# Kernel tuning notes

Hardware: AMD Instinct MI355X
Metric: run time of the kernel (lower is better)

Reference implementation:

```python
import jax, jax.numpy as jnp
import numpy as np

# ---- grid / solver constants (from opt) ----
NZ, NX = 300, 400
NPML, NPAD = 32, 0
NZP = NZ + 2 * NPML + NPAD   # 364 padded depth
NXP = NX + 2 * NPML          # 464 padded width
NSTEPS = 200
NSHOTS = 2
DX = 0.01    # km (moduli scaled by 1e-6 => velocities in km/s)
DT = 0.001   # s
SRC_Z = NPML + 2
REC_Z = NPML + 2


def _pad_model(m):
    # edge-replicate into the CPML halo + bottom pad, as ft.padding does
    return jnp.pad(m, ((NPML, NPML + NPAD), (NPML, NPML)), mode='edge')


def _sponge():
    # smooth absorbing profile in the nPml halo (sponge approximation of CPML)
    i = np.arange(NZP, dtype=np.float32)
    j = np.arange(NXP, dtype=np.float32)
    dz = np.clip(np.maximum(NPML - i, i - (NZP - 1 - NPML - NPAD)), 0, NPML) / NPML
    dx_ = np.clip(np.maximum(NPML - j, j - (NXP - 1 - NPML)), 0, NPML) / NPML
    d = dz[:, None] ** 2 + dx_[None, :] ** 2
    return jnp.asarray(np.exp(-0.1 * d), dtype=jnp.float32)


# staggered-grid finite differences (zero outside the grid)
def _dxf(f):
    return (jnp.pad(f[:, 1:], ((0, 0), (0, 1))) - f) / DX

def _dxb(f):
    return (f - jnp.pad(f[:, :-1], ((0, 0), (1, 0)))) / DX

def _dzf(f):
    return (jnp.pad(f[1:, :], ((0, 1), (0, 0))) - f) / DX

def _dzb(f):
    return (f - jnp.pad(f[:-1, :], ((1, 0), (0, 0)))) / DX


def _propagate(lam, mu, rho, stf, src_x, damp):
    """Elastic velocity-stress FDTD for one shot. stf: [NSTEPS]. Returns recs [NSTEPS, NX]."""
    lam2mu = lam + 2.0 * mu
    dt_rho = DT / rho
    zero = jnp.zeros((NZP, NXP), jnp.float32)

    def step(carry, s):
        vx, vz, sxx, szz, sxz = carry
        vx = (vx + dt_rho * (_dxf(sxx) + _dzb(sxz))) * damp
        vz = (vz + dt_rho * (_dxb(sxz) + _dzf(szz))) * damp
        dvx_dx = _dxb(vx)
        dvz_dz = _dzb(vz)
        sxx = (sxx + DT * (lam2mu * dvx_dx + lam * dvz_dz)) * damp
        szz = (szz + DT * (lam * dvx_dx + lam2mu * dvz_dz)) * damp
        sxz = (sxz + DT * mu * (_dzf(vx) + _dxf(vz))) * damp
        # explosive source injected into normal stresses
        sxx = sxx.at[SRC_Z, src_x].add(s * DT)
        szz = szz.at[SRC_Z, src_x].add(s * DT)
        rec = vx[REC_Z, NPML:NPML + NX]  # surface receiver line
        return (vx, vz, sxx, szz, sxz), rec

    init = (zero, zero, zero, zero, zero)
    _, recs = jax.lax.scan(step, init, stf)
    return recs


def _forward(Vp, Vs, Den, Stf, Mask, Shot_ids):
    Vp_pad = _pad_model(Vp)
    Vs_pad = _pad_model(Vs)
    Den_pad = _pad_model(Den)
    # masked models: gradient flows only where Mask == 1
    Vp_m = Mask * Vp_pad + (1.0 - Mask) * jax.lax.stop_gradient(Vp_pad)
    Vs_m = Mask * Vs_pad + (1.0 - Mask) * jax.lax.stop_gradient(Vs_pad)
    Den_m = Mask * Den_pad + (1.0 - Mask) * jax.lax.stop_gradient(Den_pad)
    Lam = (Vp_m ** 2 - 2.0 * Vs_m ** 2) * Den_m / 1.0e6
    Mu = Vs_m ** 2 * Den_m / 1.0e6

    damp = _sponge()
    ids = Shot_ids.astype(jnp.int32)
    src_x = NPML + 20 + ids * ((NX - 40) // NSHOTS)  # per-shot source x position
    stf = Stf[ids]                                   # [nshots, NSTEPS]
    recs = jax.vmap(lambda s, sx: _propagate(Lam, Mu, Den_m, s, sx, damp))(stf, src_x)
    return 0.5 * jnp.sum(recs.astype(jnp.float32) ** 2)  # scalar misfit


def setup_inputs() -> dict:
    key = jax.random.key(0)
    k1, k2 = jax.random.split(key)
    Vp = 2000.0 + 1500.0 * jax.random.uniform(k1, (NZ, NX), jnp.float32)   # m/s
    Vs = Vp / 1.732
    Den = 2000.0 + 500.0 * jax.random.uniform(k2, (NZ, NX), jnp.float32)   # kg/m^3
    # Ricker wavelet source, f0 = 10 Hz, shared across shots
    t = jnp.arange(NSTEPS, dtype=jnp.float32) * DT - 0.1
    f0 = 10.0
    arg = (jnp.pi * f0 * t) ** 2
    ricker = (1.0 - 2.0 * arg) * jnp.exp(-arg)
    Stf = jnp.broadcast_to(ricker, (NSHOTS, NSTEPS)).astype(jnp.float32)
    Mask = jnp.ones((NZP, NXP), jnp.float32)
    Shot_ids = jnp.arange(NSHOTS, dtype=jnp.int32)
    return {"Vp": Vp, "Vs": Vs, "Den": Den, "Stf": Stf, "Mask": Mask,
            "Shot_ids": Shot_ids, "ngpu": 1}


def reference(Vp, Vs, Den, Stf, Mask, Shot_ids, ngpu):
    return _forward(Vp, Vs, Den, Stf, Mask, Shot_ids)
```

## Files before the change

kernel.cpp:

```cpp
#include <hip/hip_runtime.h>
#include <cmath>

typedef unsigned long long u64;

namespace {
constexpr int kNZ = 300, kNX = 400;
constexpr int kNPML = 32;
constexpr int kNZP = 364, kNXP = 464;
constexpr int kNSTEPS = 200, kNSHOTS = 2;
constexpr int kSRC_Z = 34, kREC_Z = 34;
constexpr float kDT = 0.001f;
constexpr float kINV_DX = 100.0f;

constexpr int kR = 4;
constexpr int kNSLAB = 92;
constexpr int kNB = kNSLAB - 1;
constexpr int kBlocks = kNSHOTS * kNSLAB;
constexpr int kThreads = 512;
constexpr int kPitch = 468;
constexpr int kFStride = kR * kPitch;

constexpr int kFlagStride = 32;
constexpr int kHaloBase = 16384;
constexpr int kHaloCount = 2 * kNSHOTS * kNB * 2 * 6 * kNXP;
constexpr int kPartOff = kHaloBase + kHaloCount;
}

__global__ __launch_bounds__(kThreads, 1) void fwi_sim_kernel(
    const float* __restrict__ Vp, const float* __restrict__ Vs,
    const float* __restrict__ Den, const float* __restrict__ Stf,
    const int* __restrict__ Shot_ids, float* __restrict__ ws,
    float* __restrict__ out) {
    __shared__ float L[4 * kFStride];
    float* Lvx  = L;
    float* Lvz  = L + kFStride;
    float* Lsxx = L + 2 * kFStride;
    float* Lsxz = L + 3 * kFStride;

    const int blk  = blockIdx.x;
    const int s    = blk / kNSLAB;
    const int slab = blk - s * kNSLAB;
    const int r0   = slab * kR;
    const int tid  = threadIdx.x;
    const bool active = tid < kNXP;
    const int lc = tid + 1;

    int*   flags = (int*)ws;
    float* halo  = ws + kHaloBase;
    u64*   part  = (u64*)(ws + kPartOff);

    for (int q = tid; q < 4 * kFStride; q += kThreads) L[q] = 0.0f;

    auto modAt = [&](int i, int j, float& dtr_, float& dmp_, float& lam_,
                     float& mu_, float& l2m_) {
        dtr_ = dmp_ = lam_ = mu_ = l2m_ = 0.0f;
        if (i >= 0 && i < kNZP && j >= 0 && j < kNXP) {
            int iz = i - kNPML; iz = iz < 0 ? 0 : (iz > kNZ - 1 ? kNZ - 1 : iz);
            int jx = j - kNPML; jx = jx < 0 ? 0 : (jx > kNX - 1 ? kNX - 1 : jx);
            const float vp  = Vp[iz * kNX + jx];
            const float vs  = Vs[iz * kNX + jx];
            const float rho = Den[iz * kNX + jx];
            const float m = vs * vs * rho * 1e-6f;
            const float l = (vp * vp - 2.0f * vs * vs) * rho * 1e-6f;
            const float sc = kDT * kINV_DX;
            float dz = fmaxf((float)(kNPML - i), (float)(i - (kNZP - 1 - kNPML)));
            dz = fminf(fmaxf(dz, 0.0f), (float)kNPML) * (1.0f / kNPML);
            float dxx = fmaxf((float)(kNPML - j), (float)(j - (kNXP - 1 - kNPML)));
            dxx = fminf(fmaxf(dxx, 0.0f), (float)kNPML) * (1.0f / kNPML);
            dmp_ = expf(-0.1f * (dz * dz + dxx * dxx));
            dtr_ = kDT / rho * kINV_DX;
            lam_ = l * sc;
            mu_  = m * sc;
            l2m_ = (l + 2.0f * m) * sc;
        }
    };
    float rdtr[kR], rdamp[kR], rlam[kR], rmu[kR], rl2m[kR];
    float dtrT = 0, dmpT = 0, dtrB = 0, dmpB = 0;
    if (active) {
#pragma unroll
        for (int r = 0; r < kR; ++r)
            modAt(r0 + r, tid, rdtr[r], rdamp[r], rlam[r], rmu[r], rl2m[r]);
        float d0, d1, d2;
        modAt(r0 - 1, tid, dtrT, dmpT, d0, d1, d2);
        modAt(r0 + kR, tid, dtrB, dmpB, d0, d1, d2);
    }

    const int id  = Shot_ids[s];
    const int sxp = kNPML + 20 + id * ((kNX - 40) / kNSHOTS);
    const float* stf = Stf + id * kNSTEPS;
    const int rsrc = kSRC_Z - r0;
    const int rrec = kREC_Z - r0;
    const bool isRecBlock = (rrec >= 0 && rrec < kR);
    const float srcm = (active && tid == sxp) ? 1.0f : 0.0f;
    const float recm = (active && (unsigned)(tid - kNPML) < (unsigned)kNX) ? 1.0f : 0.0f;

    const bool hasTop = (slab > 0);
    const bool hasBot = (slab < kNSLAB - 1);
    int* ftopw = hasTop ? &flags[((s * kNB + (slab - 1)) * 2 + 1) * kFlagStride] : nullptr;
    int* fbotw = hasBot ? &flags[((s * kNB + slab) * 2 + 0) * kFlagStride] : nullptr;
    int* ftopr = hasTop ? &flags[((s * kNB + (slab - 1)) * 2 + 0) * kFlagStride] : nullptr;
    int* fbotr = hasBot ? &flags[((s * kNB + slab) * 2 + 1) * kFlagStride] : nullptr;
    auto hbase = [&](int buf, int b, int dir) {
        return halo + ((((buf * kNSHOTS + s) * kNB + b) * 2 + dir) * 6) * kNXP;
    };

    float fvx[kR]  = {}, fvz[kR]  = {}, fsxx[kR] = {}, fszz[kR] = {}, fsxz[kR] = {};
    float rsum = 0.0f;
    __syncthreads();

    for (int t = 0; t < kNSTEPS; ++t) {
        const int rb = (t & 1) ^ 1;
        const int wb = t & 1;

        if (active) {
#pragma unroll
            for (int r = 1; r <= kR - 2; ++r) {
                const float sxxC = fsxx[r];
                const float sxzC = fsxz[r];
                const float szzC = fszz[r];
                const float sxxR = Lsxx[r * kPitch + lc + 1];
                const float sxzL = Lsxz[r * kPitch + lc - 1];
                const float nvx = (fvx[r] + rdtr[r] * ((sxxR - sxxC) + (sxzC - fsxz[r - 1]))) * rdamp[r];
                const float nvz = (fvz[r] + rdtr[r] * ((sxzC - sxzL) + (fszz[r + 1] - szzC))) * rdamp[r];
                fvx[r] = nvx;
                fvz[r] = nvz;
                Lvx[r * kPitch + lc] = nvx;
                Lvz[r * kPitch + lc] = nvz;
                if (r == rrec) rsum += recm * nvx * nvx;
            }
        }

        if (t > 0) {
            if (hasTop) {
                while (__hip_atomic_load(ftopr, __ATOMIC_RELAXED, __HIP_MEMORY_SCOPE_AGENT) < t) {}
            }
            if (hasBot) {
                while (__hip_atomic_load(fbotr, __ATOMIC_RELAXED, __HIP_MEMORY_SCOPE_AGENT) < t) {}
            }
        }

        float h_vxT = 0, h_vzT = 0, h_sxxT = 0, h_szzT = 0, h_sxzT = 0, h_sxz2T = 0;
        float h_sxxT_r = 0, h_sxzT_l = 0;
        float h_vxB = 0, h_vzB = 0, h_sxxB = 0, h_sxzB = 0, h_szzB = 0, h_szz2B = 0;
        float h_sxxB_r = 0, h_sxzB_l = 0;
        if (t > 0 && active && hasTop) {
            const float* hb = hbase(rb, slab - 1, 0);
            h_vxT   = __hip_atomic_load(hb + tid,             __ATOMIC_RELAXED, __HIP_MEMORY_SCOPE_AGENT);
            h_vzT   = __hip_atomic_load(hb + kNXP + tid,      __ATOMIC_RELAXED, __HIP_MEMORY_SCOPE_AGENT);
            h_sxxT  = __hip_atomic_load(hb + 2 * kNXP + tid,  __ATOMIC_RELAXED, __HIP_MEMORY_SCOPE_AGENT);
            h_szzT  = __hip_atomic_load(hb + 3 * kNXP + tid,  __ATOMIC_RELAXED, __HIP_MEMORY_SCOPE_AGENT);
            h_sxzT  = __hip_atomic_load(hb + 4 * kNXP + tid,  __ATOMIC_RELAXED, __HIP_MEMORY_SCOPE_AGENT);
            h_sxz2T = __hip_atomic_load(hb + 5 * kNXP + tid,  __ATOMIC_RELAXED, __HIP_MEMORY_SCOPE_AGENT);
            if (tid < kNXP - 1) h_sxxT_r = __hip_atomic_load(hb + 2 * kNXP + tid + 1, __ATOMIC_RELAXED, __HIP_MEMORY_SCOPE_AGENT);
            if (tid > 0)        h_sxzT_l = __hip_atomic_load(hb + 4 * kNXP + tid - 1, __ATOMIC_RELAXED, __HIP_MEMORY_SCOPE_AGENT);
        }
        if (t > 0 && active && hasBot) {
            const float* hb = hbase(rb, slab, 1);
            h_vxB   = __hip_atomic_load(hb + tid,             __ATOMIC_RELAXED, __HIP_MEMORY_SCOPE_AGENT);
            h_vzB   = __hip_atomic_load(hb + kNXP + tid,      __ATOMIC_RELAXED, __HIP_MEMORY_SCOPE_AGENT);
            h_sxxB  = __hip_atomic_load(hb + 2 * kNXP + tid,  __ATOMIC_RELAXED, __HIP_MEMORY_SCOPE_AGENT);
            h_sxzB  = __hip_atomic_load(hb + 3 * kNXP + tid,  __ATOMIC_RELAXED, __HIP_MEMORY_SCOPE_AGENT);
            h_szzB  = __hip_atomic_load(hb + 4 * kNXP + tid,  __ATOMIC_RELAXED, __HIP_MEMORY_SCOPE_AGENT);
            h_szz2B = __hip_atomic_load(hb + 5 * kNXP + tid,  __ATOMIC_RELAXED, __HIP_MEMORY_SCOPE_AGENT);
            if (tid < kNXP - 1) h_sxxB_r = __hip_atomic_load(hb + 2 * kNXP + tid + 1, __ATOMIC_RELAXED, __HIP_MEMORY_SCOPE_AGENT);
            if (tid > 0)        h_sxzB_l = __hip_atomic_load(hb + 3 * kNXP + tid - 1, __ATOMIC_RELAXED, __HIP_MEMORY_SCOPE_AGENT);
        }

        float nvxT = 0, nvzT = 0, nvxB = 0, nvzB = 0;
        if (active) {
            nvxT = (h_vxT + dtrT * ((h_sxxT_r - h_sxxT) + (h_sxzT - h_sxz2T))) * dmpT;
            nvzT = (h_vzT + dtrT * ((h_sxzT - h_sxzT_l) + (fszz[0] - h_szzT))) * dmpT;
            nvxB = (h_vxB + dtrB * ((h_sxxB_r - h_sxxB) + (h_sxzB - fsxz[kR - 1]))) * dmpB;
            nvzB = (h_vzB + dtrB * ((h_sxzB - h_sxzB_l) + (h_szz2B - h_szzB))) * dmpB;
            {
                const float sxxC = fsxx[0], sxzC = fsxz[0], szzC = fszz[0];
                const float sxxR = Lsxx[lc + 1];
                const float sxzL = Lsxz[lc - 1];
                const float nvx = (fvx[0] + rdtr[0] * ((sxxR - sxxC) + (sxzC - h_sxzT))) * rdamp[0];
                const float nvz = (fvz[0] + rdtr[0] * ((sxzC - sxzL) + (fszz[1] - szzC))) * rdamp[0];
                fvx[0] = nvx; fvz[0] = nvz;
                Lvx[lc] = nvx; Lvz[lc] = nvz;
                if (0 == rrec) rsum += recm * nvx * nvx;
            }
            {
                const int r = kR - 1;
                const float sxxC = fsxx[r], sxzC = fsxz[r], szzC = fszz[r];
                const float sxxR = Lsxx[r * kPitch + lc + 1];
                const float sxzL = Lsxz[r * kPitch + lc - 1];
                const float nvx = (fvx[r] + rdtr[r] * ((sxxR - sxxC) + (sxzC - fsxz[r - 1]))) * rdamp[r];
                const float nvz = (fvz[r] + rdtr[r] * ((sxzC - sxzL) + (h_szzB - szzC))) * rdamp[r];
                fvx[r] = nvx; fvz[r] = nvz;
                Lvx[r * kPitch + lc] = nvx; Lvz[r * kPitch + lc] = nvz;
                if (r == rrec) rsum += recm * nvx * nvx;
            }
        }
        __syncthreads();

        if (active) {
            const float sval = stf[t] * kDT;
#pragma unroll
            for (int r = 0; r < kR; ++r) {
                const float vxC = fvx[r];
                const float vzC = fvz[r];
                const float vxL = Lvx[r * kPitch + lc - 1];
                const float vzR = Lvz[r * kPitch + lc + 1];
                const float vzU = (r > 0) ? fvz[r - 1] : nvzT;
                const float vxD = (r < kR - 1) ? fvx[r + 1] : nvxB;
                const float dvx = vxC - vxL;
                const float dvz = vzC - vzU;
                float nsxx = (fsxx[r] + (rl2m[r] * dvx + rlam[r] * dvz)) * rdamp[r];
                float nszz = (fszz[r] + (rlam[r] * dvx + rl2m[r] * dvz)) * rdamp[r];
                float nsxz = (fsxz[r] + rmu[r] * ((vxD - vxC) + (vzR - vzC))) * rdamp[r];
                if (r == rsrc) { nsxx += srcm * sval; nszz += srcm * sval; }
                fsxx[r] = nsxx;
                fszz[r] = nszz;
                fsxz[r] = nsxz;
                Lsxx[r * kPitch + lc] = nsxx;
                Lsxz[r * kPitch + lc] = nsxz;
            }
            if (hasTop) {
                float* hb = hbase(wb, slab - 1, 1);
                __hip_atomic_store(hb + tid,            fvx[0],  __ATOMIC_RELAXED, __HIP_MEMORY_SCOPE_AGENT);
                __hip_atomic_store(hb + kNXP + tid,     fvz[0],  __ATOMIC_RELAXED, __HIP_MEMORY_SCOPE_AGENT);
                __hip_atomic_store(hb + 2 * kNXP + tid, fsxx[0], __ATOMIC_RELAXED, __HIP_MEMORY_SCOPE_AGENT);
                __hip_atomic_store(hb + 3 * kNXP + tid, fsxz[0], __ATOMIC_RELAXED, __HIP_MEMORY_SCOPE_AGENT);
                __hip_atomic_store(hb + 4 * kNXP + tid, fszz[0], __ATOMIC_RELAXED, __HIP_MEMORY_SCOPE_AGENT);
                __hip_atomic_store(hb + 5 * kNXP + tid, fszz[1], __ATOMIC_RELAXED, __HIP_MEMORY_SCOPE_AGENT);
            }
            if (hasBot) {
                float* hb = hbase(wb, slab, 0);
                __hip_atomic_store(hb + tid,            fvx[kR - 1],  __ATOMIC_RELAXED, __HIP_MEMORY_SCOPE_AGENT);
                __hip_atomic_store(hb + kNXP + tid,     fvz[kR - 1],  __ATOMIC_RELAXED, __HIP_MEMORY_SCOPE_AGENT);
                __hip_atomic_store(hb + 2 * kNXP + tid, fsxx[kR - 1], __ATOMIC_RELAXED, __HIP_MEMORY_SCOPE_AGENT);
                __hip_atomic_store(hb + 3 * kNXP + tid, fszz[kR - 1], __ATOMIC_RELAXED, __HIP_MEMORY_SCOPE_AGENT);
                __hip_atomic_store(hb + 4 * kNXP + tid, fsxz[kR - 1], __ATOMIC_RELAXED, __HIP_MEMORY_SCOPE_AGENT);
                __hip_atomic_store(hb + 5 * kNXP + tid, fsxz[kR - 2], __ATOMIC_RELAXED, __HIP_MEMORY_SCOPE_AGENT);
            }
        }
        __syncthreads();
        if (tid == 0 && hasTop) __hip_atomic_store(ftopw, t + 1, __ATOMIC_RELAXED, __HIP_MEMORY_SCOPE_AGENT);
        if (tid == 1 && hasBot) __hip_atomic_store(fbotw, t + 1, __ATOMIC_RELAXED, __HIP_MEMORY_SCOPE_AGENT);
    }

    for (int off = 32; off > 0; off >>= 1) rsum += __shfl_down(rsum, off, 64);
    __syncthreads();
    if ((tid & 63) == 0) L[tid >> 6] = rsum;
    __syncthreads();
    if (isRecBlock && tid == 0) {
        float tot = 0.0f;
#pragma unroll
        for (int w = 0; w < kThreads / 64; ++w) tot += L[w];
        const u64 word = ((u64)1 << 32) | (u64)__float_as_uint(tot);
        __hip_atomic_store(&part[s], word, __ATOMIC_RELAXED, __HIP_MEMORY_SCOPE_AGENT);
    }
    if (blk == 0 && tid == 0) {
        u64 v0, v1;
        do { v0 = __hip_atomic_load(&part[0], __ATOMIC_RELAXED, __HIP_MEMORY_SCOPE_AGENT); }
        while ((int)(v0 >> 32) < 1);
        do { v1 = __hip_atomic_load(&part[1], __ATOMIC_RELAXED, __HIP_MEMORY_SCOPE_AGENT); }
        while ((int)(v1 >> 32) < 1);
        out[0] = 0.5f * (__uint_as_float((unsigned)v0) + __uint_as_float((unsigned)v1));
    }
}

extern "C" void kernel_launch(void* const* d_in, const int* in_sizes, int n_in,
                              void* d_out, int out_size, void* d_ws, size_t ws_size,
                              hipStream_t stream) {
    const float* Vp  = (const float*)d_in[0];
    const float* Vs  = (const float*)d_in[1];
    const float* Den = (const float*)d_in[2];
    const float* Stf = (const float*)d_in[3];
    const int* Shot_ids = (const int*)d_in[5];
    float* out = (float*)d_out;
    float* ws  = (float*)d_ws;

    fwi_sim_kernel<<<kBlocks, kThreads, 0, stream>>>(Vp, Vs, Den, Stf,
                                                     Shot_ids, ws, out);
}
```

Baseline: 604.8 us.

## Overlap interior velocity update with halo publish and use lighter barriers

The interior-row velocity update for the next step now runs after the stress phase and before the flag publish, so it overlaps the latency of the halo stores. Boundary stress rows are computed first so halo stores issue earlier. __syncthreads is replaced by inline-asm barriers that wait only on LDS counters, with a vmcnt drain before the flags are signalled. The per-neighbour flag wait is also interleaved with that neighbour's halo loads. The risk is memory-ordering correctness, since the code relies on hand-written waitcnt plus relaxed atomics.

```diff
diff --git a/kernel.cpp b/kernel.cpp
--- a/kernel.cpp
+++ b/kernel.cpp
@@ -25,6 +25,42 @@
 constexpr int kHaloCount = 2 * kNSHOTS * kNB * 2 * 6 * kNXP;
 constexpr int kPartOff = kHaloBase + kHaloCount;
 }
+
+#define ALD(p)    __hip_atomic_load((p),       __ATOMIC_RELAXED, __HIP_MEMORY_SCOPE_AGENT)
+#define AST(p, v) __hip_atomic_store((p), (v), __ATOMIC_RELAXED, __HIP_MEMORY_SCOPE_AGENT)
+#define LDS_BAR() asm volatile("s_waitcnt lgkmcnt(0)\n\ts_barrier" ::: "memory")
+#define DRAIN_BAR() asm volatile("s_waitcnt vmcnt(0)\n\ts_barrier" ::: "memory")
+
+#define PRE_VEL()                                                              \
+  if (active) {                                                                \
+    _Pragma("unroll")                                                          \
+    for (int r = 1; r <= kR - 2; ++r) {                                        \
+      const float sxxC = fsxx[r], sxzC = fsxz[r], szzC = fszz[r];              \
+      const float sxxR = Lsxx[r * kPitch + lc + 1];                            \
+      const float sxzL = Lsxz[r * kPitch + lc - 1];                            \
+      const float nvx = (fvx[r] + rdtr[r] * ((sxxR - sxxC) + (sxzC - fsxz[r - 1]))) * rdamp[r]; \
+      const float nvz = (fvz[r] + rdtr[r] * ((sxzC - sxzL) + (fszz[r + 1] - szzC))) * rdamp[r]; \
+      fvx[r] = nvx; fvz[r] = nvz;                                              \
+      Lvx[r * kPitch + lc] = nvx; Lvz[r * kPitch + lc] = nvz;                  \
+      if (r == rrec) rsum += recm * nvx * nvx;                                 \
+    }                                                                          \
+  }
+
+#define STRESS_ROW(r, VZU, VXD)                                                \
+  {                                                                            \
+    const float vxC = fvx[r], vzC = fvz[r];                                    \
+    const float vxL = Lvx[(r) * kPitch + lc - 1];                              \
+    const float vzR = Lvz[(r) * kPitch + lc + 1];                              \
+    const float dvx = vxC - vxL;                                               \
+    const float dvz = vzC - (VZU);                                             \
+    float nsxx = (fsxx[r] + (rl2m[r] * dvx + rlam[r] * dvz)) * rdamp[r];       \
+    float nszz = (fszz[r] + (rlam[r] * dvx + rl2m[r] * dvz)) * rdamp[r];       \
+    float nsxz = (fsxz[r] + rmu[r] * (((VXD) - vxC) + (vzR - vzC))) * rdamp[r];\
+    if ((r) == rsrc) { nsxx += srcm * sval; nszz += srcm * sval; }             \
+    fsxx[r] = nsxx; fszz[r] = nszz; fsxz[r] = nsxz;                            \
+    Lsxx[(r) * kPitch + lc] = nsxx;                                            \
+    Lsxz[(r) * kPitch + lc] = nsxz;                                            \
+  }
 
 __global__ __launch_bounds__(kThreads, 1) void fwi_sim_kernel(
     const float* __restrict__ Vp, const float* __restrict__ Vs,
@@ -108,70 +144,51 @@
     float rsum = 0.0f;
     __syncthreads();
 
+    PRE_VEL()
+
     for (int t = 0; t < kNSTEPS; ++t) {
         const int rb = (t & 1) ^ 1;
         const int wb = t & 1;
-
-        if (active) {
-#pragma unroll
-            for (int r = 1; r <= kR - 2; ++r) {
-                const float sxxC = fsxx[r];
-                const float sxzC = fsxz[r];
-                const float szzC = fszz[r];
-                const float sxxR = Lsxx[r * kPitch + lc + 1];
-                const float sxzL = Lsxz[r * kPitch + lc - 1];
-                const float nvx = (fvx[r] + rdtr[r] * ((sxxR - sxxC) + (sxzC - fsxz[r - 1]))) * rdamp[r];
-                const float nvz = (fvz[r] + rdtr[r] * ((sxzC - sxzL) + (fszz[r + 1] - szzC))) * rdamp[r];
-                fvx[r] = nvx;
-                fvz[r] = nvz;
-                Lvx[r * kPitch + lc] = nvx;
-                Lvz[r * kPitch + lc] = nvz;
-                if (r == rrec) rsum += recm * nvx * nvx;
-            }
-        }
-
-        if (t > 0) {
-            if (hasTop) {
-                while (__hip_atomic_load(ftopr, __ATOMIC_RELAXED, __HIP_MEMORY_SCOPE_AGENT) < t) {}
-            }
-            if (hasBot) {
-                while (__hip_atomic_load(fbotr, __ATOMIC_RELAXED, __HIP_MEMORY_SCOPE_AGENT) < t) {}
-            }
-        }
 
         float h_vxT = 0, h_vzT = 0, h_sxxT = 0, h_szzT = 0, h_sxzT = 0, h_sxz2T = 0;
         float h_sxxT_r = 0, h_sxzT_l = 0;
         float h_vxB = 0, h_vzB = 0, h_sxxB = 0, h_sxzB = 0, h_szzB = 0, h_szz2B = 0;
         float h_sxxB_r = 0, h_sxzB_l = 0;
-        if (t > 0 && active && hasTop) {
-            const float* hb = hbase(rb, slab - 1, 0);
-            h_vxT   = __hip_atomic_load(hb + tid,             __ATOMIC_RELAXED, __HIP_MEMORY_SCOPE_AGENT);
-            h_vzT   = __hip_atomic_load(hb + kNXP + tid,      __ATOMIC_RELAXED, __HIP_MEMORY_SCOPE_AGENT);
-            h_sxxT  = __hip_atomic_load(hb + 2 * kNXP + tid,  __ATOMIC_RELAXED, __HIP_MEMORY_SCOPE_AGENT);
-            h_szzT  = __hip_atomic_load(hb + 3 * kNXP + tid,  __ATOMIC_RELAXED, __HIP_MEMORY_SCOPE_AGENT);
-            h_sxzT  = __hip_atomic_load(hb + 4 * kNXP + tid,  __ATOMIC_RELAXED, __HIP_MEMORY_SCOPE_AGENT);
-            h_sxz2T = __hip_atomic_load(hb + 5 * kNXP + tid,  __ATOMIC_RELAXED, __HIP_MEMORY_SCOPE_AGENT);
-            if (tid < kNXP - 1) h_sxxT_r = __hip_atomic_load(hb + 2 * kNXP + tid + 1, __ATOMIC_RELAXED, __HIP_MEMORY_SCOPE_AGENT);
-            if (tid > 0)        h_sxzT_l = __hip_atomic_load(hb + 4 * kNXP + tid - 1, __ATOMIC_RELAXED, __HIP_MEMORY_SCOPE_AGENT);
-        }
-        if (t > 0 && active && hasBot) {
-            const float* hb = hbase(rb, slab, 1);
-            h_vxB   = __hip_atomic_load(hb + tid,             __ATOMIC_RELAXED, __HIP_MEMORY_SCOPE_AGENT);
-            h_vzB   = __hip_atomic_load(hb + kNXP + tid,      __ATOMIC_RELAXED, __HIP_MEMORY_SCOPE_AGENT);
-            h_sxxB  = __hip_atomic_load(hb + 2 * kNXP + tid,  __ATOMIC_RELAXED, __HIP_MEMORY_SCOPE_AGENT);
-            h_sxzB  = __hip_atomic_load(hb + 3 * kNXP + tid,  __ATOMIC_RELAXED, __HIP_MEMORY_SCOPE_AGENT);
-            h_szzB  = __hip_atomic_load(hb + 4 * kNXP + tid,  __ATOMIC_RELAXED, __HIP_MEMORY_SCOPE_AGENT);
-            h_szz2B = __hip_atomic_load(hb + 5 * kNXP + tid,  __ATOMIC_RELAXED, __HIP_MEMORY_SCOPE_AGENT);
-            if (tid < kNXP - 1) h_sxxB_r = __hip_atomic_load(hb + 2 * kNXP + tid + 1, __ATOMIC_RELAXED, __HIP_MEMORY_SCOPE_AGENT);
-            if (tid > 0)        h_sxzB_l = __hip_atomic_load(hb + 3 * kNXP + tid - 1, __ATOMIC_RELAXED, __HIP_MEMORY_SCOPE_AGENT);
+        if (t > 0) {
+            if (hasTop) {
+                while (ALD(ftopr) < t) {}
+                if (active) {
+                    const float* hb = hbase(rb, slab - 1, 0);
+                    h_vxT   = ALD(hb + tid);
+                    h_vzT   = ALD(hb + kNXP + tid);
+                    h_sxxT  = ALD(hb + 2 * kNXP + tid);
+                    h_szzT  = ALD(hb + 3 * kNXP + tid);
+                    h_sxzT  = ALD(hb + 4 * kNXP + tid);
+                    h_sxz2T = ALD(hb + 5 * kNXP + tid);
+                    if (tid < kNXP - 1) h_sxxT_r = ALD(hb + 2 * kNXP + tid + 1);
+                    if (tid > 0)        h_sxzT_l = ALD(hb + 4 * kNXP + tid - 1);
+                }
+            }
+            if (hasBot) {
+                while (ALD(fbotr) < t) {}
+                if (active) {
+                    const float* hb = hbase(rb, slab, 1);
+                    h_vxB   = ALD(hb + tid);
+                    h_vzB   = ALD(hb + kNXP + tid);
+                    h_sxxB  = ALD(hb + 2 * kNXP + tid);
+                    h_sxzB  = ALD(hb + 3 * kNXP + tid);
+                    h_szzB  = ALD(hb + 4 * kNXP + tid);
+                    h_szz2B = ALD(hb + 5 * kNXP + tid);
+                    if (tid < kNXP - 1) h_sxxB_r = ALD(hb + 2 * kNXP + tid + 1);
+                    if (tid > 0)        h_sxzB_l = ALD(hb + 3 * kNXP + tid - 1);
+                }
+            }
         }
 
         float nvxT = 0, nvzT = 0, nvxB = 0, nvzB = 0;
         if (active) {
             nvxT = (h_vxT + dtrT * ((h_sxxT_r - h_sxxT) + (h_sxzT - h_sxz2T))) * dmpT;
             nvzT = (h_vzT + dtrT * ((h_sxzT - h_sxzT_l) + (fszz[0] - h_szzT))) * dmpT;
-            nvxB = (h_vxB + dtrB * ((h_sxxB_r - h_sxxB) + (h_sxzB - fsxz[kR - 1]))) * dmpB;
-            nvzB = (h_vzB + dtrB * ((h_sxzB - h_sxzB_l) + (h_szz2B - h_szzB))) * dmpB;
             {
                 const float sxxC = fsxx[0], sxzC = fsxz[0], szzC = fszz[0];
                 const float sxxR = Lsxx[lc + 1];
@@ -182,6 +199,8 @@
                 Lvx[lc] = nvx; Lvz[lc] = nvz;
                 if (0 == rrec) rsum += recm * nvx * nvx;
             }
+            nvxB = (h_vxB + dtrB * ((h_sxxB_r - h_sxxB) + (h_sxzB - fsxz[kR - 1]))) * dmpB;
+            nvzB = (h_vzB + dtrB * ((h_sxzB - h_sxzB_l) + (h_szz2B - h_szzB))) * dmpB;
             {
                 const int r = kR - 1;
                 const float sxxC = fsxx[r], sxzC = fsxz[r], szzC = fszz[r];
@@ -194,52 +213,40 @@
                 if (r == rrec) rsum += recm * nvx * nvx;
             }
         }
-        __syncthreads();
+        LDS_BAR();
 
         if (active) {
             const float sval = stf[t] * kDT;
-#pragma unroll
-            for (int r = 0; r < kR; ++r) {
-                const float vxC = fvx[r];
-                const float vzC = fvz[r];
-                const float vxL = Lvx[r * kPitch + lc - 1];
-                const float vzR = Lvz[r * kPitch + lc + 1];
-                const float vzU = (r > 0) ? fvz[r - 1] : nvzT;
-                const float vxD = (r < kR - 1) ? fvx[r + 1] : nvxB;
-                const float dvx = vxC - vxL;
-                const float dvz = vzC - vzU;
-                float nsxx = (fsxx[r] + (rl2m[r] * dvx + rlam[r] * dvz)) * rdamp[r];
-                float nszz = (fszz[r] + (rlam[r] * dvx + rl2m[r] * dvz)) * rdamp[r];
-                float nsxz = (fsxz[r] + rmu[r] * ((vxD - vxC) + (vzR - vzC))) * rdamp[r];
-                if (r == rsrc) { nsxx += srcm * sval; nszz += srcm * sval; }
-                fsxx[r] = nsxx;
-                fszz[r] = nszz;
-                fsxz[r] = nsxz;
-                Lsxx[r * kPitch + lc] = nsxx;
-                Lsxz[r * kPitch + lc] = nsxz;
-            }
+            STRESS_ROW(0, nvzT, fvx[1])
+            STRESS_ROW(1, fvz[0], fvx[2])
             if (hasTop) {
                 float* hb = hbase(wb, slab - 1, 1);
-                __hip_atomic_store(hb + tid,            fvx[0],  __ATOMIC_RELAXED, __HIP_MEMORY_SCOPE_AGENT);
-                __hip_atomic_store(hb + kNXP + tid,     fvz[0],  __ATOMIC_RELAXED, __HIP_MEMORY_SCOPE_AGENT);
-                __hip_atomic_store(hb + 2 * kNXP + tid, fsxx[0], __ATOMIC_RELAXED, __HIP_MEMORY_SCOPE_AGENT);
-                __hip_atomic_store(hb + 3 * kNXP + tid, fsxz[0], __ATOMIC_RELAXED, __HIP_MEMORY_SCOPE_AGENT);
-                __hip_atomic_store(hb + 4 * kNXP + tid, fszz[0], __ATOMIC_RELAXED, __HIP_MEMORY_SCOPE_AGENT);
-                __hip_atomic_store(hb + 5 * kNXP + tid, fszz[1], __ATOMIC_RELAXED, __HIP_MEMORY_SCOPE_AGENT);
-            }
+                AST(hb + tid,            fvx[0]);
+                AST(hb + kNXP + tid,     fvz[0]);
+                AST(hb + 2 * kNXP + tid, fsxx[0]);
+                AST(hb + 3 * kNXP + tid, fsxz[0]);
+                AST(hb + 4 * kNXP + tid, fszz[0]);
+                AST(hb + 5 * kNXP + tid, fszz[1]);
+            }
+            STRESS_ROW(3, fvz[2], nvxB)
+            STRESS_ROW(2, fvz[1], fvx[3])
             if (hasBot) {
                 float* hb = hbase(wb, slab, 0);
-                __hip_atomic_store(hb + tid,            fvx[kR - 1],  __ATOMIC_RELAXED, __HIP_MEMORY_SCOPE_AGENT);
-                __hip_atomic_store(hb + kNXP + tid,     fvz[kR - 1],  __ATOMIC_RELAXED, __HIP_MEMORY_SCOPE_AGENT);
-                __hip_atomic_store(hb + 2 * kNXP + tid, fsxx[kR - 1], __ATOMIC_RELAXED, __HIP_MEMORY_SCOPE_AGENT);
-                __hip_atomic_store(hb + 3 * kNXP + tid, fszz[kR - 1], __ATOMIC_RELAXED, __HIP_MEMORY_SCOPE_AGENT);
-                __hip_atomic_store(hb + 4 * kNXP + tid, fsxz[kR - 1], __ATOMIC_RELAXED, __HIP_MEMORY_SCOPE_AGENT);
-                __hip_atomic_store(hb + 5 * kNXP + tid, fsxz[kR - 2], __ATOMIC_RELAXED, __HIP_MEMORY_SCOPE_AGENT);
-            }
-        }
-        __syncthreads();
-        if (tid == 0 && hasTop) __hip_atomic_store(ftopw, t + 1, __ATOMIC_RELAXED, __HIP_MEMORY_SCOPE_AGENT);
-        if (tid == 1 && hasBot) __hip_atomic_store(fbotw, t + 1, __ATOMIC_RELAXED, __HIP_MEMORY_SCOPE_AGENT);
+                AST(hb + tid,            fvx[kR - 1]);
+                AST(hb + kNXP + tid,     fvz[kR - 1]);
+                AST(hb + 2 * kNXP + tid, fsxx[kR - 1]);
+                AST(hb + 3 * kNXP + tid, fszz[kR - 1]);
+                AST(hb + 4 * kNXP + tid, fsxz[kR - 1]);
+                AST(hb + 5 * kNXP + tid, fsxz[kR - 2]);
+            }
+        }
+        LDS_BAR();
+
+        if (t + 1 < kNSTEPS) { PRE_VEL() }
+
+        DRAIN_BAR();
+        if (tid == 0 && hasTop) AST(ftopw, t + 1);
+        if (tid == 1 && hasBot) AST(fbotw, t + 1);
     }
 
     for (int off = 32; off > 0; off >>= 1) rsum += __shfl_down(rsum, off, 64);
@@ -251,14 +258,12 @@
 #pragma unroll
         for (int w = 0; w < kThreads / 64; ++w) tot += L[w];
         const u64 word = ((u64)1 << 32) | (u64)__float_as_uint(tot);
-        __hip_atomic_store(&part[s], word, __ATOMIC_RELAXED, __HIP_MEMORY_SCOPE_AGENT);
+        AST(&part[s], word);
     }
     if (blk == 0 && tid == 0) {
         u64 v0, v1;
-        do { v0 = __hip_atomic_load(&part[0], __ATOMIC_RELAXED, __HIP_MEMORY_SCOPE_AGENT); }
-        while ((int)(v0 >> 32) < 1);
-        do { v1 = __hip_atomic_load(&part[1], __ATOMIC_RELAXED, __HIP_MEMORY_SCOPE_AGENT); }
-        while ((int)(v1 >> 32) < 1);
+        do { v0 = ALD(&part[0]); } while ((int)(v0 >> 32) < 1);
+        do { v1 = ALD(&part[1]); } while ((int)(v1 >> 32) < 1);
         out[0] = 0.5f * (__uint_as_float((unsigned)v0) + __uint_as_float((unsigned)v1));
     }
 }
```

After: 736.6 us. 21.8% more time.
